# Kernel tuning notes

Measured on AMD Instinct MI355X. Metric: run time of the kernel, lower is better.

Reference implementation:

```python
import jax, jax.numpy as jnp
import numpy as np

C = 512
H = 8
D = C // H
GROUPS = 32
EPS = 1e-5

def setup_inputs() -> dict:
    key = jax.random.key(0)
    ks = jax.random.split(key, 7)
    B, L = 4, 2048
    x = jax.random.normal(ks[0], (B, C, L), dtype=jnp.float32)
    gamma = jnp.ones((C,), dtype=jnp.float32)
    beta = jnp.zeros((C,), dtype=jnp.float32)
    w_qkv = jax.random.normal(ks[1], (3 * C, C), dtype=jnp.float32) * (1.0 / np.sqrt(C))
    b_qkv = jax.random.normal(ks[2], (3 * C,), dtype=jnp.float32) * 0.01
    w_proj = jax.random.normal(ks[3], (C, C), dtype=jnp.float32) * (1.0 / np.sqrt(C))
    b_proj = jax.random.normal(ks[4], (C,), dtype=jnp.float32) * 0.01
    return {"x": x, "gamma": gamma, "beta": beta, "w_qkv": w_qkv,
            "b_qkv": b_qkv, "w_proj": w_proj, "b_proj": b_proj}

def _group_norm(x, gamma, beta):
    B, Cc, L = x.shape
    xg = x.reshape(B, GROUPS, Cc // GROUPS, L)
    mean = jnp.mean(xg, axis=(2, 3), keepdims=True)
    var = jnp.var(xg, axis=(2, 3), keepdims=True)
    xn = ((xg - mean) * jax.lax.rsqrt(var + EPS)).reshape(B, Cc, L)
    return xn * gamma[None, :, None] + beta[None, :, None]

def reference(x, gamma, beta, w_qkv, b_qkv, w_proj, b_proj):
    B, Cc, L = x.shape
    h = _group_norm(x, gamma, beta)
    # 1x1 conv == channel matmul: (3C,C) x (B,C,L) -> (B,3C,L)
    qkv = jnp.einsum('oc,bcl->bol', w_qkv, h) + b_qkv[None, :, None]
    q, k, v = jnp.split(qkv, 3, axis=1)
    # (B,C,L) -> (B,H,L,D)
    def to_heads(t):
        return t.reshape(B, H, D, L).transpose(0, 1, 3, 2)
    q, k, v = to_heads(q), to_heads(k), to_heads(v)
    scale = 1.0 / np.sqrt(D).astype(np.float32)
    attn = jnp.einsum('bhqd,bhkd->bhqk', q, k) * scale  # [B,H,L,L]
    attn = jax.nn.softmax(attn, axis=-1)
    out = jnp.einsum('bhqk,bhkd->bhqd', attn, v)  # [B,H,L,D]
    out = out.transpose(0, 1, 3, 2).reshape(B, Cc, L)
    proj = jnp.einsum('oc,bcl->bol', w_proj, out) + b_proj[None, :, None]
    return x + proj
```

## Files before the change

kernel.cpp:

```cpp
#include <hip/hip_runtime.h>
#include <stdint.h>

#define C_DIM 512
#define H_HEADS 8
#define D_HEAD 64
#define B_BATCH 4
#define L_SEQ 2048
#define GROUPS 32
#define EPS_GN 1e-5f

typedef unsigned short u16;
typedef __attribute__((ext_vector_type(8))) __bf16 bf16x8;
typedef __attribute__((ext_vector_type(4))) float f32x4;
typedef __attribute__((ext_vector_type(16))) float f32x16;

__device__ __forceinline__ u16 f2bf(float f) {
  unsigned u = __builtin_bit_cast(unsigned, f);
  unsigned r = u + 0x7FFFu + ((u >> 16) & 1u);
  return (u16)(r >> 16);
}

__device__ __forceinline__ unsigned cvtpk_bf16(float lo, float hi) {
  unsigned r;
  asm("v_cvt_pk_bf16_f32 %0, %1, %2" : "=v"(r) : "v"(lo), "v"(hi));
  return r;
}

__device__ __forceinline__ void pl32swap(unsigned& a, unsigned& b) {
  asm("v_permlane32_swap_b32 %0, %1" : "+v"(a), "+v"(b));
}

__device__ __forceinline__ bf16x8 mk8(unsigned a, unsigned b, unsigned c, unsigned d) {
  union { uint4 u; bf16x8 v; } z;
  z.u.x = a; z.u.y = b; z.u.z = c; z.u.w = d;
  return z.v;
}

__device__ __forceinline__ void gl16(const void* g, void* l) {
  __builtin_amdgcn_global_load_lds((const __attribute__((address_space(1))) void*)g,
                                   (__attribute__((address_space(3))) void*)l, 16, 0, 0);
}

__global__ __launch_bounds__(256) void cvt_weights(const float* __restrict__ wq,
                                                   const float* __restrict__ wp,
                                                   u16* __restrict__ wq_bf,
                                                   u16* __restrict__ wp_bf) {
  int i = blockIdx.x * 256 + threadIdx.x;
  const int nq = 3 * C_DIM * C_DIM;
  int idx = i * 4;
  const float* src;
  u16* dst;
  if (idx < nq) { src = wq + idx; dst = wq_bf + idx; }
  else          { src = wp + (idx - nq); dst = wp_bf + (idx - nq); }
  float4 v = *(const float4*)src;
  uint2 pk;
  pk.x = (unsigned)f2bf(v.x) | ((unsigned)f2bf(v.y) << 16);
  pk.y = (unsigned)f2bf(v.z) | ((unsigned)f2bf(v.w) << 16);
  *(uint2*)dst = pk;
}

__global__ __launch_bounds__(256) void groupnorm_kernel(const float* __restrict__ x,
                                                        const float* __restrict__ gamma,
                                                        const float* __restrict__ beta,
                                                        u16* __restrict__ h_t) {
  int bg = blockIdx.x;
  int b = bg >> 5, g = bg & 31;
  const float* base = x + ((size_t)(b * C_DIM + g * 16)) * L_SEQ;
  int t = threadIdx.x;
  int w = t >> 6;
  float s = 0.f, sq = 0.f;
  for (int i = 0; i < 32; ++i) {
    float4 v = ((const float4*)base)[t + i * 256];
    s += v.x + v.y + v.z + v.w;
    sq += v.x * v.x + v.y * v.y + v.z * v.z + v.w * v.w;
  }
  for (int off = 32; off; off >>= 1) { s += __shfl_down(s, off); sq += __shfl_down(sq, off); }
  __shared__ float red[8];
  if ((t & 63) == 0) { red[w * 2] = s; red[w * 2 + 1] = sq; }
  __syncthreads();
  float ts = red[0] + red[2] + red[4] + red[6];
  float tq = red[1] + red[3] + red[5] + red[7];
  float mean = ts * (1.f / 32768.f);
  float var = tq * (1.f / 32768.f) - mean * mean;
  float rstd = rsqrtf(var + EPS_GN);
  float ga[16], be[16];
#pragma unroll
  for (int c = 0; c < 16; ++c) {
    float gm = gamma[g * 16 + c];
    ga[c] = gm * rstd;
    be[c] = beta[g * 16 + c] - mean * gm * rstd;
  }
  __shared__ float tile[16][260];
  for (int lc = 0; lc < 8; ++lc) {
    __syncthreads();
#pragma unroll
    for (int it = 0; it < 4; ++it) {
      int r = it * 4 + w;
      int c4 = (t & 63) * 4;
      *(float4*)&tile[r][c4] = *(const float4*)(base + (size_t)r * L_SEQ + lc * 256 + c4);
    }
    __syncthreads();
    int l = lc * 256 + t;
    unsigned wds[8];
#pragma unroll
    for (int c = 0; c < 8; ++c) {
      float a0 = tile[2 * c][t] * ga[2 * c] + be[2 * c];
      float a1 = tile[2 * c + 1][t] * ga[2 * c + 1] + be[2 * c + 1];
      wds[c] = (unsigned)f2bf(a0) | ((unsigned)f2bf(a1) << 16);
    }
    u16* dst = h_t + ((size_t)(b * L_SEQ + l)) * C_DIM + g * 16;
    uint4 p0; p0.x = wds[0]; p0.y = wds[1]; p0.z = wds[2]; p0.w = wds[3];
    uint4 p1; p1.x = wds[4]; p1.y = wds[5]; p1.z = wds[6]; p1.w = wds[7];
    *(uint4*)dst = p0;
    *(uint4*)(dst + 8) = p1;
  }
}

template <int MODE>
__global__ __launch_bounds__(256) void gemm_kernel(const u16* __restrict__ A_bf,
                                                   const u16* __restrict__ B_t,
                                                   const float* __restrict__ bias,
                                                   const float* __restrict__ xres,
                                                   u16* __restrict__ q_t,
                                                   u16* __restrict__ kf_g,
                                                   u16* __restrict__ vf_g,
                                                   float* __restrict__ out_f) {
  constexpr int K = 512;
  __shared__ u16 A_lds[128][32];
  __shared__ u16 B_lds[128][32];
  int t = threadIdx.x;
  int w = t >> 6, lane = t & 63;
  int q4 = lane >> 4, c15 = lane & 15;
  int wm = w >> 1, wn = w & 1;
  int o0 = blockIdx.y * 128;
  int l0 = blockIdx.x * 128;
  int b = blockIdx.z;
  const u16* Bb = B_t + (size_t)b * L_SEQ * K;
  f32x4 acc[4][4] = {};

  int sr = lane >> 2, sc = lane & 3;
  int r0 = w * 32 + sr;
  int r1 = r0 + 16;
  int lc0 = (sc - (r0 >> 1)) & 3;
  int lc1 = (sc - (r1 >> 1)) & 3;
  const u16* Ag0 = A_bf + (size_t)(o0 + r0) * K + lc0 * 8;
  const u16* Ag1 = A_bf + (size_t)(o0 + r1) * K + lc1 * 8;
  const u16* Bg0 = Bb + (size_t)(l0 + r0) * K + lc0 * 8;
  const u16* Bg1 = Bb + (size_t)(l0 + r1) * K + lc1 * 8;
  u16* Al0 = &A_lds[w * 32][0];
  u16* Al1 = &A_lds[w * 32 + 16][0];
  u16* Bl0 = &B_lds[w * 32][0];
  u16* Bl1 = &B_lds[w * 32 + 16][0];

  for (int kt = 0; kt < K / 32; ++kt) {
    gl16(Ag0, Al0); gl16(Ag1, Al1);
    gl16(Bg0, Bl0); gl16(Bg1, Bl1);
    Ag0 += 32; Ag1 += 32; Bg0 += 32; Bg1 += 32;
    __syncthreads();
    bf16x8 af[4], bfr[4];
#pragma unroll
    for (int mi = 0; mi < 4; ++mi) {
      int ar = wm * 64 + mi * 16 + c15;
      af[mi] = *(const bf16x8*)&A_lds[ar][((q4 + (ar >> 1)) & 3) * 8];
    }
#pragma unroll
    for (int ni = 0; ni < 4; ++ni) {
      int br = wn * 64 + ni * 16 + c15;
      bfr[ni] = *(const bf16x8*)&B_lds[br][((q4 + (br >> 1)) & 3) * 8];
    }
#pragma unroll
    for (int mi = 0; mi < 4; ++mi)
#pragma unroll
      for (int ni = 0; ni < 4; ++ni)
        acc[mi][ni] = __builtin_amdgcn_mfma_f32_16x16x32_bf16(af[mi], bfr[ni], acc[mi][ni], 0, 0, 0);
    __syncthreads();
  }

  if (MODE == 0) {
    const float QS = 0.18033688f;
    int sel = o0 >> 9;
    int ob = o0 - sel * 512 + wm * 64;
#pragma unroll
    for (int mi = 0; mi < 4; ++mi) {
      int orow = ob + mi * 16 + q4 * 4;
      float4 bi = *(const float4*)&bias[o0 + wm * 64 + mi * 16 + q4 * 4];
#pragma unroll
      for (int ni = 0; ni < 4; ++ni) {
        int l = l0 + wn * 64 + ni * 16 + c15;
        float v0 = acc[mi][ni][0] + bi.x;
        float v1 = acc[mi][ni][1] + bi.y;
        float v2 = acc[mi][ni][2] + bi.z;
        float v3 = acc[mi][ni][3] + bi.w;
        if (sel == 0) {
          v0 *= QS; v1 *= QS; v2 *= QS; v3 *= QS;
          uint2 pk;
          pk.x = (unsigned)f2bf(v0) | ((unsigned)f2bf(v1) << 16);
          pk.y = (unsigned)f2bf(v2) | ((unsigned)f2bf(v3) << 16);
          *(uint2*)(q_t + ((size_t)(b * L_SEQ + l)) * C_DIM + orow) = pk;
        } else if (sel == 1) {
          int hh = orow >> 6, d = orow & 63;
          size_t base = ((size_t)(b * 8 + hh)) * 131072 +
                        (size_t)(((l >> 5) * 4 + (d >> 4))) * 512 +
                        (size_t)((l & 31) + ((d >> 3) & 1) * 32) * 8 + (d & 7);
          uint2 pk;
          pk.x = (unsigned)f2bf(v0) | ((unsigned)f2bf(v1) << 16);
          pk.y = (unsigned)f2bf(v2) | ((unsigned)f2bf(v3) << 16);
          *(uint2*)(kf_g + base) = pk;
        } else {
          int hh = orow >> 6, d = orow & 63;
          size_t base0 = ((size_t)(b * 8 + hh)) * 131072 +
                         (size_t)(l >> 4) * 1024 +
                         (size_t)((l >> 3) & 1) * 256 + (l & 7);
          vf_g[base0 + (size_t)((d + 0) >> 5) * 512 + ((d + 0) & 31) * 8] = f2bf(v0);
          vf_g[base0 + (size_t)((d + 1) >> 5) * 512 + ((d + 1) & 31) * 8] = f2bf(v1);
          vf_g[base0 + (size_t)((d + 2) >> 5) * 512 + ((d + 2) & 31) * 8] = f2bf(v2);
          vf_g[base0 + (size_t)((d + 3) >> 5) * 512 + ((d + 3) & 31) * 8] = f2bf(v3);
        }
      }
    }
  } else {
#pragma unroll
    for (int mi = 0; mi < 4; ++mi) {
      int orow = o0 + wm * 64 + mi * 16 + q4 * 4;
      float4 bi = *(const float4*)&bias[orow];
#pragma unroll
      for (int ni = 0; ni < 4; ++ni) {
        int l = l0 + wn * 64 + ni * 16 + c15;
        size_t base2 = ((size_t)(b * C_DIM + orow)) * L_SEQ + l;
        out_f[base2] = acc[mi][ni][0] + bi.x + xres[base2];
        out_f[base2 + L_SEQ] = acc[mi][ni][1] + bi.y + xres[base2 + L_SEQ];
        out_f[base2 + 2 * L_SEQ] = acc[mi][ni][2] + bi.z + xres[base2 + 2 * L_SEQ];
        out_f[base2 + 3 * L_SEQ] = acc[mi][ni][3] + bi.w + xres[base2 + 3 * L_SEQ];
      }
    }
  }
}

#define ABODY(KL, KN, VC, SC, SN, T)                                           \
  {                                                                            \
    int tl = (T) + 2; tl = tl > 63 ? 63 : tl;                                  \
    const u16* kp = kfb + tl * 2048;                                           \
    const u16* vp = vfb + tl * 2048;                                           \
    KL[0] = *(const bf16x8*)(kp);                                              \
    KL[1] = *(const bf16x8*)(kp + 512);                                        \
    KL[2] = *(const bf16x8*)(kp + 1024);                                       \
    KL[3] = *(const bf16x8*)(kp + 1536);                                       \
    _Pragma("unroll") for (int r = 0; r < 16; ++r) SN[r] = 0.f;                \
    _Pragma("unroll") for (int kk = 0; kk < 4; ++kk)                           \
        SN = __builtin_amdgcn_mfma_f32_32x32x16_bf16(KN[kk], qf[kk], SN, 0, 0, 0); \
    float mx = fmaxf(fmaxf(SC[0], SC[1]), SC[2]);                              \
    float m1 = fmaxf(fmaxf(SC[3], SC[4]), SC[5]);                              \
    float m2 = fmaxf(fmaxf(SC[6], SC[7]), SC[8]);                              \
    float m3 = fmaxf(fmaxf(SC[9], SC[10]), SC[11]);                            \
    float m4 = fmaxf(fmaxf(SC[12], SC[13]), SC[14]);                           \
    mx = fmaxf(fmaxf(mx, SC[15]), fmaxf(m1, m2));                              \
    mx = fmaxf(mx, fmaxf(m3, m4));                                             \
    mx = fmaxf(mx, __shfl_xor(mx, 32));                                        \
    if (__any(mx > m_r + 8.f)) {                                               \
      float mnew = fmaxf(m_r, mx);                                             \
      float al = __builtin_amdgcn_exp2f(m_r - mnew);                           \
      l_r *= al;                                                               \
      _Pragma("unroll") for (int r = 0; r < 16; ++r) { o0[r] *= al; o1[r] *= al; } \
      m_r = mnew;                                                              \
    }                                                                          \
    _Pragma("unroll") for (int r = 0; r < 16; ++r)                             \
        SC[r] = __builtin_amdgcn_exp2f(SC[r] - m_r);                           \
    float s0 = (SC[0] + SC[1]) + (SC[2] + SC[3]);                              \
    float s1 = (SC[4] + SC[5]) + (SC[6] + SC[7]);                              \
    float s2 = (SC[8] + SC[9]) + (SC[10] + SC[11]);                            \
    float s3 = (SC[12] + SC[13]) + (SC[14] + SC[15]);                          \
    float sum = (s0 + s1) + (s2 + s3);                                         \
    sum += __shfl_xor(sum, 32);                                                \
    l_r += sum;                                                                \
    unsigned pk[8];                                                            \
    _Pragma("unroll") for (int i = 0; i < 8; ++i)                              \
        pk[i] = cvtpk_bf16(SC[2 * i], SC[2 * i + 1]);                          \
    pl32swap(pk[0], pk[2]); pl32swap(pk[1], pk[3]);                            \
    pl32swap(pk[4], pk[6]); pl32swap(pk[5], pk[7]);                            \
    bf16x8 pf0 = mk8(pk[0], pk[1], pk[2], pk[3]);                              \
    bf16x8 pf1 = mk8(pk[4], pk[5], pk[6], pk[7]);                              \
    o0 = __builtin_amdgcn_mfma_f32_32x32x16_bf16(VC[0], pf0, o0, 0, 0, 0);     \
    o1 = __builtin_amdgcn_mfma_f32_32x32x16_bf16(VC[1], pf0, o1, 0, 0, 0);     \
    o0 = __builtin_amdgcn_mfma_f32_32x32x16_bf16(VC[2], pf1, o0, 0, 0, 0);     \
    o1 = __builtin_amdgcn_mfma_f32_32x32x16_bf16(VC[3], pf1, o1, 0, 0, 0);     \
    VC[0] = *(const bf16x8*)(vp);                                              \
    VC[1] = *(const bf16x8*)(vp + 512);                                        \
    VC[2] = *(const bf16x8*)(vp + 1024);                                       \
    VC[3] = *(const bf16x8*)(vp + 1536);                                       \
  }

#define AEPI(VC, SC)                                                           \
  {                                                                            \
    float mx = fmaxf(fmaxf(SC[0], SC[1]), SC[2]);                              \
    float m1 = fmaxf(fmaxf(SC[3], SC[4]), SC[5]);                              \
    float m2 = fmaxf(fmaxf(SC[6], SC[7]), SC[8]);                              \
    float m3 = fmaxf(fmaxf(SC[9], SC[10]), SC[11]);                            \
    float m4 = fmaxf(fmaxf(SC[12], SC[13]), SC[14]);                           \
    mx = fmaxf(fmaxf(mx, SC[15]), fmaxf(m1, m2));                              \
    mx = fmaxf(mx, fmaxf(m3, m4));                                             \
    mx = fmaxf(mx, __shfl_xor(mx, 32));                                        \
    if (__any(mx > m_r + 8.f)) {                                               \
      float mnew = fmaxf(m_r, mx);                                             \
      float al = __builtin_amdgcn_exp2f(m_r - mnew);                           \
      l_r *= al;                                                               \
      _Pragma("unroll") for (int r = 0; r < 16; ++r) { o0[r] *= al; o1[r] *= al; } \
      m_r = mnew;                                                              \
    }                                                                          \
    _Pragma("unroll") for (int r = 0; r < 16; ++r)                             \
        SC[r] = __builtin_amdgcn_exp2f(SC[r] - m_r);                           \
    float s0 = (SC[0] + SC[1]) + (SC[2] + SC[3]);                              \
    float s1 = (SC[4] + SC[5]) + (SC[6] + SC[7]);                              \
    float s2 = (SC[8] + SC[9]) + (SC[10] + SC[11]);                            \
    float s3 = (SC[12] + SC[13]) + (SC[14] + SC[15]);                          \
    float sum = (s0 + s1) + (s2 + s3);                                         \
    sum += __shfl_xor(sum, 32);                                                \
    l_r += sum;                                                                \
    unsigned pk[8];                                                            \
    _Pragma("unroll") for (int i = 0; i < 8; ++i)                              \
        pk[i] = cvtpk_bf16(SC[2 * i], SC[2 * i + 1]);                          \
    pl32swap(pk[0], pk[2]); pl32swap(pk[1], pk[3]);                            \
    pl32swap(pk[4], pk[6]); pl32swap(pk[5], pk[7]);                            \
    bf16x8 pf0 = mk8(pk[0], pk[1], pk[2], pk[3]);                              \
    bf16x8 pf1 = mk8(pk[4], pk[5], pk[6], pk[7]);                              \
    o0 = __builtin_amdgcn_mfma_f32_32x32x16_bf16(VC[0], pf0, o0, 0, 0, 0);     \
    o1 = __builtin_amdgcn_mfma_f32_32x32x16_bf16(VC[1], pf0, o1, 0, 0, 0);     \
    o0 = __builtin_amdgcn_mfma_f32_32x32x16_bf16(VC[2], pf1, o0, 0, 0, 0);     \
    o1 = __builtin_amdgcn_mfma_f32_32x32x16_bf16(VC[3], pf1, o1, 0, 0, 0);     \
  }

__global__ __launch_bounds__(256, 2) void attn_kernel(const u16* __restrict__ q_t,
                                                      const u16* __restrict__ kf_g,
                                                      const u16* __restrict__ vf_g,
                                                      u16* __restrict__ ao_t) {
  int g = blockIdx.x;
  int wk = (g & 7) * 64 + (g >> 3);
  int qb = wk & 15, bh = wk >> 4;
  int b = bh >> 3, h = bh & 7;
  int t = threadIdx.x;
  int wv = t >> 6, lane = t & 63;
  int q = lane & 31, hi = lane >> 5;
  int q0 = qb * 128 + wv * 32;

  const u16* qp = q_t + ((size_t)(b * L_SEQ + q0 + q)) * C_DIM + h * 64 + hi * 8;
  bf16x8 qf[4];
#pragma unroll
  for (int kk = 0; kk < 4; ++kk) qf[kk] = *(const bf16x8*)(qp + kk * 16);

  const u16* kfb = kf_g + (size_t)bh * 131072 + lane * 8;
  const u16* vfb = vf_g + (size_t)bh * 131072 + lane * 8;

  f32x16 o0, o1;
#pragma unroll
  for (int r = 0; r < 16; ++r) { o0[r] = 0.f; o1[r] = 0.f; }
  float m_r = -1e30f, l_r = 0.f;

  bf16x8 kA[4], kB[4], vA[4], vB[4];
#pragma unroll
  for (int i = 0; i < 4; ++i) {
    kB[i] = *(const bf16x8*)(kfb + i * 512);
    kA[i] = *(const bf16x8*)(kfb + 2048 + i * 512);
    vA[i] = *(const bf16x8*)(vfb + i * 512);
    vB[i] = *(const bf16x8*)(vfb + 2048 + i * 512);
  }
  f32x16 sA, sB;
#pragma unroll
  for (int r = 0; r < 16; ++r) sA[r] = 0.f;
#pragma unroll
  for (int kk = 0; kk < 4; ++kk)
    sA = __builtin_amdgcn_mfma_f32_32x32x16_bf16(kB[kk], qf[kk], sA, 0, 0, 0);

  for (int it = 0; it < 31; ++it) {
    ABODY(kB, kA, vA, sA, sB, 2 * it);
    ABODY(kA, kB, vB, sB, sA, 2 * it + 1);
  }
  ABODY(kB, kA, vA, sA, sB, 62);
  AEPI(vB, sB);

  float inv = 1.f / l_r;
  u16* dst = ao_t + ((size_t)(b * L_SEQ + q0 + q)) * C_DIM + h * 64;
#pragma unroll
  for (int tq = 0; tq < 4; ++tq) {
    uint2 w0, w1;
    w0.x = cvtpk_bf16(o0[4 * tq] * inv, o0[4 * tq + 1] * inv);
    w0.y = cvtpk_bf16(o0[4 * tq + 2] * inv, o0[4 * tq + 3] * inv);
    *(uint2*)(dst + 8 * tq + 4 * hi) = w0;
    w1.x = cvtpk_bf16(o1[4 * tq] * inv, o1[4 * tq + 1] * inv);
    w1.y = cvtpk_bf16(o1[4 * tq + 2] * inv, o1[4 * tq + 3] * inv);
    *(uint2*)(dst + 32 + 8 * tq + 4 * hi) = w1;
  }
}

extern "C" void kernel_launch(void* const* d_in, const int* in_sizes, int n_in,
                              void* d_out, int out_size, void* d_ws, size_t ws_size,
                              hipStream_t stream) {
  const float* x = (const float*)d_in[0];
  const float* gamma = (const float*)d_in[1];
  const float* beta = (const float*)d_in[2];
  const float* w_qkv = (const float*)d_in[3];
  const float* b_qkv = (const float*)d_in[4];
  const float* w_proj = (const float*)d_in[5];
  const float* b_proj = (const float*)d_in[6];
  float* out = (float*)d_out;

  u16* wq_bf = (u16*)d_ws;
  u16* wp_bf = wq_bf + 786432;
  u16* h_t = wp_bf + 262144;
  u16* q_t = h_t + 4194304;
  u16* kf_g = q_t + 4194304;
  u16* vf_g = kf_g + 4194304;
  u16* ao_t = vf_g + 4194304;

  cvt_weights<<<dim3(1024), dim3(256), 0, stream>>>(w_qkv, w_proj, wq_bf, wp_bf);
  groupnorm_kernel<<<dim3(128), dim3(256), 0, stream>>>(x, gamma, beta, h_t);
  gemm_kernel<0><<<dim3(16, 12, 4), dim3(256), 0, stream>>>(wq_bf, h_t, b_qkv, nullptr, q_t, kf_g, vf_g, nullptr);
  attn_kernel<<<dim3(512), dim3(256), 0, stream>>>(q_t, kf_g, vf_g, ao_t);
  gemm_kernel<1><<<dim3(16, 4, 4), dim3(256), 0, stream>>>(wp_bf, ao_t, b_proj, x, nullptr, nullptr, nullptr, out);
}
```

Baseline: 112.4 us.

## Split attention KV range across waves and merge partial softmax via shared memory

Each block now handles 32 queries, and its four waves each process a quarter of the key/value sequence (split-K flash attention). The per-wave partial max, sum and output are combined through shared memory before one coalesced bf16 store. The grid grows from 512 to 2048 blocks and launch bounds ask for 3 blocks per CU, to fill the GPU better and shorten each wave's serial loop. The lazy, threshold-gated rescale is replaced by an unconditional rescale on every tile. The cost is extra shared memory and barriers, repeated Q loads, and more exp/multiply work per tile.

```diff
diff --git a/kernel.cpp b/kernel.cpp
--- a/kernel.cpp
+++ b/kernel.cpp
@@ -238,7 +238,7 @@
 
 #define ABODY(KL, KN, VC, SC, SN, T)                                           \
   {                                                                            \
-    int tl = (T) + 2; tl = tl > 63 ? 63 : tl;                                  \
+    int tl = (T) + 2; tl = tl > TMAX ? TMAX : tl;                              \
     const u16* kp = kfb + tl * 2048;                                           \
     const u16* vp = vfb + tl * 2048;                                           \
     KL[0] = *(const bf16x8*)(kp);                                              \
@@ -256,13 +256,11 @@
     mx = fmaxf(fmaxf(mx, SC[15]), fmaxf(m1, m2));                              \
     mx = fmaxf(mx, fmaxf(m3, m4));                                             \
     mx = fmaxf(mx, __shfl_xor(mx, 32));                                        \
-    if (__any(mx > m_r + 8.f)) {                                               \
-      float mnew = fmaxf(m_r, mx);                                             \
-      float al = __builtin_amdgcn_exp2f(m_r - mnew);                           \
-      l_r *= al;                                                               \
-      _Pragma("unroll") for (int r = 0; r < 16; ++r) { o0[r] *= al; o1[r] *= al; } \
-      m_r = mnew;                                                              \
-    }                                                                          \
+    float mnew = fmaxf(m_r, mx);                                               \
+    float al = __builtin_amdgcn_exp2f(m_r - mnew);                             \
+    m_r = mnew;                                                                \
+    l_r *= al;                                                                 \
+    _Pragma("unroll") for (int r = 0; r < 16; ++r) { o0[r] *= al; o1[r] *= al; } \
     _Pragma("unroll") for (int r = 0; r < 16; ++r)                             \
         SC[r] = __builtin_amdgcn_exp2f(SC[r] - m_r);                           \
     float s0 = (SC[0] + SC[1]) + (SC[2] + SC[3]);                              \
@@ -299,13 +297,11 @@
     mx = fmaxf(fmaxf(mx, SC[15]), fmaxf(m1, m2));                              \
     mx = fmaxf(mx, fmaxf(m3, m4));                                             \
     mx = fmaxf(mx, __shfl_xor(mx, 32));                                        \
-    if (__any(mx > m_r + 8.f)) {                                               \
-      float mnew = fmaxf(m_r, mx);                                             \
-      float al = __builtin_amdgcn_exp2f(m_r - mnew);                           \
-      l_r *= al;                                                               \
-      _Pragma("unroll") for (int r = 0; r < 16; ++r) { o0[r] *= al; o1[r] *= al; } \
-      m_r = mnew;                                                              \
-    }                                                                          \
+    float mnew = fmaxf(m_r, mx);                                               \
+    float al = __builtin_amdgcn_exp2f(m_r - mnew);                             \
+    m_r = mnew;                                                                \
+    l_r *= al;                                                                 \
+    _Pragma("unroll") for (int r = 0; r < 16; ++r) { o0[r] *= al; o1[r] *= al; } \
     _Pragma("unroll") for (int r = 0; r < 16; ++r)                             \
         SC[r] = __builtin_amdgcn_exp2f(SC[r] - m_r);                           \
     float s0 = (SC[0] + SC[1]) + (SC[2] + SC[3]);                              \
@@ -328,26 +324,31 @@
     o1 = __builtin_amdgcn_mfma_f32_32x32x16_bf16(VC[3], pf1, o1, 0, 0, 0);     \
   }
 
-__global__ __launch_bounds__(256, 2) void attn_kernel(const u16* __restrict__ q_t,
+__global__ __launch_bounds__(256, 3) void attn_kernel(const u16* __restrict__ q_t,
                                                       const u16* __restrict__ kf_g,
                                                       const u16* __restrict__ vf_g,
                                                       u16* __restrict__ ao_t) {
+  __shared__ float oL[4][64][32];
+  __shared__ float mL[4][32];
+  __shared__ float lL[4][32];
+
   int g = blockIdx.x;
-  int wk = (g & 7) * 64 + (g >> 3);
-  int qb = wk & 15, bh = wk >> 4;
+  int wk = (g & 7) * 256 + (g >> 3);
+  int qg = wk & 63, bh = wk >> 6;
   int b = bh >> 3, h = bh & 7;
   int t = threadIdx.x;
   int wv = t >> 6, lane = t & 63;
   int q = lane & 31, hi = lane >> 5;
-  int q0 = qb * 128 + wv * 32;
+  int q0 = qg * 32;
+  const int TMAX = 15;
 
   const u16* qp = q_t + ((size_t)(b * L_SEQ + q0 + q)) * C_DIM + h * 64 + hi * 8;
   bf16x8 qf[4];
 #pragma unroll
   for (int kk = 0; kk < 4; ++kk) qf[kk] = *(const bf16x8*)(qp + kk * 16);
 
-  const u16* kfb = kf_g + (size_t)bh * 131072 + lane * 8;
-  const u16* vfb = vf_g + (size_t)bh * 131072 + lane * 8;
+  const u16* kfb = kf_g + (size_t)bh * 131072 + (size_t)wv * 32768 + lane * 8;
+  const u16* vfb = vf_g + (size_t)bh * 131072 + (size_t)wv * 32768 + lane * 8;
 
   f32x16 o0, o1;
 #pragma unroll
@@ -369,25 +370,42 @@
   for (int kk = 0; kk < 4; ++kk)
     sA = __builtin_amdgcn_mfma_f32_32x32x16_bf16(kB[kk], qf[kk], sA, 0, 0, 0);
 
-  for (int it = 0; it < 31; ++it) {
+  for (int it = 0; it < 7; ++it) {
     ABODY(kB, kA, vA, sA, sB, 2 * it);
     ABODY(kA, kB, vB, sB, sA, 2 * it + 1);
   }
-  ABODY(kB, kA, vA, sA, sB, 62);
+  ABODY(kB, kA, vA, sA, sB, 14);
   AEPI(vB, sB);
 
-  float inv = 1.f / l_r;
-  u16* dst = ao_t + ((size_t)(b * L_SEQ + q0 + q)) * C_DIM + h * 64;
-#pragma unroll
-  for (int tq = 0; tq < 4; ++tq) {
-    uint2 w0, w1;
-    w0.x = cvtpk_bf16(o0[4 * tq] * inv, o0[4 * tq + 1] * inv);
-    w0.y = cvtpk_bf16(o0[4 * tq + 2] * inv, o0[4 * tq + 3] * inv);
-    *(uint2*)(dst + 8 * tq + 4 * hi) = w0;
-    w1.x = cvtpk_bf16(o1[4 * tq] * inv, o1[4 * tq + 1] * inv);
-    w1.y = cvtpk_bf16(o1[4 * tq + 2] * inv, o1[4 * tq + 3] * inv);
-    *(uint2*)(dst + 32 + 8 * tq + 4 * hi) = w1;
-  }
+  if (hi == 0) mL[wv][q] = m_r;
+  __syncthreads();
+  float ms = fmaxf(fmaxf(mL[0][q], mL[1][q]), fmaxf(mL[2][q], mL[3][q]));
+  float scl = __builtin_amdgcn_exp2f(m_r - ms);
+  if (hi == 0) lL[wv][q] = l_r * scl;
+#pragma unroll
+  for (int r = 0; r < 16; ++r) {
+    int d = (r & 3) + 8 * (r >> 2) + 4 * hi;
+    oL[wv][d][q] = o0[r] * scl;
+    oL[wv][d + 32][q] = o1[r] * scl;
+  }
+  __syncthreads();
+
+  int tq = t & 31;
+  int dbase = (t >> 5) * 8;
+  float lsum = (lL[0][tq] + lL[1][tq]) + (lL[2][tq] + lL[3][tq]);
+  float inv = 1.f / lsum;
+  float v[8];
+#pragma unroll
+  for (int i = 0; i < 8; ++i) {
+    int d = dbase + i;
+    v[i] = ((oL[0][d][tq] + oL[1][d][tq]) + (oL[2][d][tq] + oL[3][d][tq])) * inv;
+  }
+  uint4 ov;
+  ov.x = cvtpk_bf16(v[0], v[1]);
+  ov.y = cvtpk_bf16(v[2], v[3]);
+  ov.z = cvtpk_bf16(v[4], v[5]);
+  ov.w = cvtpk_bf16(v[6], v[7]);
+  *(uint4*)(ao_t + ((size_t)(b * L_SEQ + q0 + tq)) * C_DIM + h * 64 + dbase) = ov;
 }
 
 extern "C" void kernel_launch(void* const* d_in, const int* in_sizes, int n_in,
@@ -413,6 +431,6 @@
   cvt_weights<<<dim3(1024), dim3(256), 0, stream>>>(w_qkv, w_proj, wq_bf, wp_bf);
   groupnorm_kernel<<<dim3(128), dim3(256), 0, stream>>>(x, gamma, beta, h_t);
   gemm_kernel<0><<<dim3(16, 12, 4), dim3(256), 0, stream>>>(wq_bf, h_t, b_qkv, nullptr, q_t, kf_g, vf_g, nullptr);
-  attn_kernel<<<dim3(512), dim3(256), 0, stream>>>(q_t, kf_g, vf_g, ao_t);
+  attn_kernel<<<dim3(2048), dim3(256), 0, stream>>>(q_t, kf_g, vf_g, ao_t);
   gemm_kernel<1><<<dim3(16, 4, 4), dim3(256), 0, stream>>>(wp_bf, ao_t, b_proj, x, nullptr, nullptr, nullptr, out);
 }
```

Result: slower. 116.8 us (+4.0%).
